# Optimization experiments

Measured on AMD Instinct MI355X. Metric: run time of the kernel, lower is better.

Reference implementation:

```python
import jax, jax.numpy as jnp
import numpy as np

B, L, DIN = 32, 512, 768
H, DH = 16, 48
DOUT = H * DH
NEG = 1e12


def setup_inputs() -> dict:
    key = jax.random.key(0)
    ks = jax.random.split(key, 8)
    lim = float(np.sqrt(6.0 / (DIN + DOUT)))  # xavier_uniform
    return {
        "Q_seq": jax.random.normal(ks[0], (B, L, DIN), jnp.float32),
        "K_seq": jax.random.normal(ks[1], (B, L, DIN), jnp.float32),
        "V_seq": jax.random.normal(ks[2], (B, L, DIN), jnp.float32),
        "WQ": jax.random.uniform(ks[3], (DIN, DOUT), jnp.float32, -lim, lim),
        "WK": jax.random.uniform(ks[4], (DIN, DOUT), jnp.float32, -lim, lim),
        "WV": jax.random.uniform(ks[5], (DIN, DOUT), jnp.float32, -lim, lim),
        "Q_len": jax.random.randint(ks[6], (B, 1), 0, L, jnp.int64),
        "V_len": jax.random.randint(ks[7], (B, 1), 0, L, jnp.int64),
    }


def reference(Q_seq, K_seq, V_seq, WQ, WK, WV, Q_len, V_len):
    b, l = Q_seq.shape[0], Q_seq.shape[1]
    # projections -> [B, H, L, DH]
    q = (Q_seq @ WQ).reshape(b, l, H, DH).transpose(0, 2, 1, 3)
    k = (K_seq @ WK).reshape(b, l, H, DH).transpose(0, 2, 1, 3)
    v = (V_seq @ WV).reshape(b, l, H, DH).transpose(0, 2, 1, 3)
    # scaled scores [B, H, Lq, Lk]
    A = jnp.einsum("bhqd,bhkd->bhqk", q, k) / jnp.sqrt(jnp.float32(DH))
    # key-length additive mask (original: scatter+cumsum == arange < len)
    mask_k = (jnp.arange(l) < V_len[:, 0][:, None]).astype(A.dtype)  # [B, Lk]
    A = A - (1.0 - mask_k)[:, None, None, :] * NEG
    # causal mask (mask_right=True): subtract on strictly upper triangle
    A = A - jnp.triu(jnp.ones((l, l), A.dtype), 1) * NEG
    A = jax.nn.softmax(A, axis=-1)
    # original quirk: O = A^T @ V  -> O[b,h,k,d] = sum_q A[b,h,q,k] V[b,h,q,d]
    O = jnp.einsum("bhqk,bhqd->bkhd", A, v).reshape(b, l, DOUT)
    # query-length multiplicative mask on output
    mask_q = (jnp.arange(l) < Q_len[:, 0][:, None]).astype(O.dtype)  # [B, L]
    return O * mask_q[:, :, None]
```

## Files before the change

kernel.cpp:

```cpp
#include <hip/hip_runtime.h>
#include <stdint.h>

#define B_    32
#define L_    512
#define DIN_  768
#define H_    16
#define DH_   48
#define DOUT_ 768
#define NHEADS (B_ * H_)
#define HEADELEMS (L_ * DH_)

typedef short bf16x8 __attribute__((ext_vector_type(8)));
typedef float f32x4  __attribute__((ext_vector_type(4)));

__device__ __forceinline__ uint16_t f2bf(float f) {
  uint32_t u = __float_as_uint(f);
  u += 0x7fffu + ((u >> 16) & 1u);
  return (uint16_t)(u >> 16);
}
__device__ __forceinline__ uint32_t pack2bf(float lo, float hi) {
  uint32_t a = __float_as_uint(lo);
  a += 0x7fffu + ((a >> 16) & 1u);
  uint32_t b = __float_as_uint(hi);
  b += 0x7fffu + ((b >> 16) & 1u);
  return (a >> 16) | (b & 0xffff0000u);
}
__device__ __forceinline__ void gload_lds16(const void* g, void* l) {
  __builtin_amdgcn_global_load_lds(
      (const __attribute__((address_space(1))) uint32_t*)g,
      (__attribute__((address_space(3))) uint32_t*)l, 16, 0, 0);
}
__device__ __forceinline__ bf16x8 lds_frag8(const uint16_t* p) {
  union { uint2 u[2]; bf16x8 v; } x;
  x.u[0] = *(const uint2*)(p);
  x.u[1] = *(const uint2*)(p + 4);
  return x.v;
}

__global__ void lens_kernel(const int* __restrict__ qlen_raw,
                            const int* __restrict__ vlen_raw,
                            int* __restrict__ lens) {
  __shared__ int is64[2];
  int t = threadIdx.x;
  if (t < 2) {
    const int* src = (t == 0) ? qlen_raw : vlen_raw;
    int o = 0;
    for (int i = 0; i < 16; ++i) o |= src[2 * i + 1];
    is64[t] = (o == 0) ? 1 : 0;
  }
  __syncthreads();
  int which = t >> 5;
  int i = t & 31;
  const int* src = which ? vlen_raw : qlen_raw;
  lens[t] = is64[which] ? src[2 * i] : src[i];
}

__global__ void wconv_kernel(const float* __restrict__ WQ,
                             const float* __restrict__ WK,
                             const float* __restrict__ WV,
                             uint16_t* __restrict__ Wt) {
  const int z = blockIdx.z;
  const float* W = (z == 0) ? WQ : (z == 1) ? WK : WV;
  uint16_t* dst = Wt + (size_t)z * DIN_ * DOUT_;
  const int n  = blockIdx.x * 256 + threadIdx.x;
  const int k4 = blockIdx.y * 4;
  float f0 = W[(size_t)(k4 + 0) * DOUT_ + n];
  float f1 = W[(size_t)(k4 + 1) * DOUT_ + n];
  float f2 = W[(size_t)(k4 + 2) * DOUT_ + n];
  float f3 = W[(size_t)(k4 + 3) * DOUT_ + n];
  uint2 p;
  p.x = pack2bf(f0, f1);
  p.y = pack2bf(f2, f3);
  *(uint2*)&dst[(size_t)n * DIN_ + k4] = p;
}

__global__ __launch_bounds__(512, 4) void mfma_proj(
    const float* __restrict__ Xq, const float* __restrict__ Xk,
    const float* __restrict__ Xv, const uint16_t* __restrict__ Wt,
    uint16_t* __restrict__ qh, uint16_t* __restrict__ kh,
    uint16_t* __restrict__ vh) {
  const int z = blockIdx.z;
  const float* X = (z == 0) ? Xq : (z == 1) ? Xk : Xv;
  uint16_t* dst  = (z == 0) ? qh : (z == 1) ? kh : vh;
  const uint16_t* W = Wt + (size_t)z * DIN_ * DOUT_;

  __shared__ uint16_t As[128][32];
  __shared__ uint16_t Bs[128][32];

  const int t  = threadIdx.x;
  const int m0 = blockIdx.x * 128;
  const int n0 = blockIdx.y * 128;

  const int ra = t >> 2;
  const int ca = (t & 3) * 8;
  const float* aptr = X + (size_t)(m0 + ra) * DIN_ + ca;

  const uint16_t* bptr = W + (size_t)(n0 + (t >> 2)) * DIN_ + (t & 3) * 8;
  void* ldsB = (char*)(&Bs[0][0]) + t * 16;

  const int w = t >> 6, lane = t & 63;
  const int wm = (w & 3) * 32, wn = (w >> 2) * 64;
  const int fr = lane & 15;
  const int quad = lane >> 4;

  f32x4 acc[2][4];
#pragma unroll
  for (int i = 0; i < 2; ++i)
#pragma unroll
    for (int j = 0; j < 4; ++j) acc[i][j] = f32x4{0.f, 0.f, 0.f, 0.f};

  for (int kt = 0; kt < DIN_ / 32; ++kt) {
    const int k0 = kt * 32;
    gload_lds16(bptr + k0, ldsB);
    float4 x0 = *(const float4*)(aptr + k0);
    float4 x1 = *(const float4*)(aptr + k0 + 4);
    uint4 pA;
    pA.x = pack2bf(x0.x, x0.y); pA.y = pack2bf(x0.z, x0.w);
    pA.z = pack2bf(x1.x, x1.y); pA.w = pack2bf(x1.z, x1.w);
    *(uint4*)&As[ra][ca] = pA;
    __syncthreads();

    bf16x8 af[2], bfr[4];
#pragma unroll
    for (int i = 0; i < 2; ++i)
      af[i]  = *(const bf16x8*)&As[wm + i * 16 + fr][quad * 8];
#pragma unroll
    for (int j = 0; j < 4; ++j)
      bfr[j] = *(const bf16x8*)&Bs[wn + j * 16 + fr][quad * 8];
#pragma unroll
    for (int mt = 0; mt < 2; ++mt)
#pragma unroll
      for (int nt = 0; nt < 4; ++nt)
        acc[mt][nt] = __builtin_amdgcn_mfma_f32_16x16x32_bf16(
            af[mt], bfr[nt], acc[mt][nt], 0, 0, 0);
    __syncthreads();
  }

#pragma unroll
  for (int mt = 0; mt < 2; ++mt) {
#pragma unroll
    for (int r = 0; r < 4; ++r) {
      const int m  = m0 + wm + mt * 16 + quad * 4 + r;
      const int bb = m >> 9;
      const int l  = m & 511;
#pragma unroll
      for (int nt = 0; nt < 4; ++nt) {
        const int n = n0 + wn + nt * 16 + fr;
        const int h = n / DH_;
        const int d = n - h * DH_;
        dst[(((size_t)bb * H_ + h) * L_ + l) * DH_ + d] = f2bf(acc[mt][nt][r]);
      }
    }
  }
}

__global__ __launch_bounds__(256, 2) void attn_mfma(
    const uint16_t* __restrict__ qh, const uint16_t* __restrict__ kh,
    const uint16_t* __restrict__ vh, const int* __restrict__ lens,
    float* __restrict__ out) {
  const int bh = blockIdx.x;
  const int b  = bh >> 4;
  const int h  = bh & 15;
  const int t    = threadIdx.x;
  const int w    = t >> 6;
  const int lane = t & 63;
  const int l15  = lane & 15;
  const int quad = lane >> 4;

  const int qlen = lens[b];
  const int vlen = lens[32 + b];
  const bool deg = (vlen == 0);
  const size_t head = (size_t)bh * HEADELEMS;

  __shared__ uint16_t Pt[4][128][36];
  __shared__ uint16_t Vt[48][36];
  __shared__ float    prt[4][32];
  __shared__ float    cmb[32];

  const uint16_t* qbase = qh + head;
  const uint16_t* kbase = kh + head;
  const uint16_t* vbase = vh + head;

  f32x4 Oacc[8][3];
#pragma unroll
  for (int i = 0; i < 8; ++i)
#pragma unroll
    for (int dt = 0; dt < 3; ++dt) Oacc[i][dt] = f32x4{0.f, 0.f, 0.f, 0.f};

  const float scale = 0.14433756729740643f;
  const int vq  = t & 31;
  const int vd4 = t >> 5;

  for (int g = 0; g < 16; ++g) {
    const int q0 = g * 32;
    const int lim = q0 + 31 - 16 * w;

    __syncthreads();

    {
      uint2 u = *(const uint2*)(vbase + (size_t)(q0 + vq) * DH_ + vd4 * 4);
      Vt[vd4 * 4 + 0][vq] = (uint16_t)(u.x);
      Vt[vd4 * 4 + 1][vq] = (uint16_t)(u.x >> 16);
      Vt[vd4 * 4 + 2][vq] = (uint16_t)(u.y);
      Vt[vd4 * 4 + 3][vq] = (uint16_t)(u.y >> 16);
      if (t < 128) {
        int d4b = 8 + (t >> 5);
        uint2 v = *(const uint2*)(vbase + (size_t)(q0 + vq) * DH_ + d4b * 4);
        Vt[d4b * 4 + 0][vq] = (uint16_t)(v.x);
        Vt[d4b * 4 + 1][vq] = (uint16_t)(v.x >> 16);
        Vt[d4b * 4 + 2][vq] = (uint16_t)(v.y);
        Vt[d4b * 4 + 3][vq] = (uint16_t)(v.y >> 16);
      }
    }

    bf16x8 aq[2][2];
#pragma unroll
    for (int mt = 0; mt < 2; ++mt) {
      const uint16_t* qp = qbase + (size_t)(q0 + mt * 16 + l15) * DH_;
      aq[mt][0] = *(const bf16x8*)(qp + quad * 8);
      bf16x8 zz = {0, 0, 0, 0, 0, 0, 0, 0};
      aq[mt][1] = zz;
      if (quad < 2) aq[mt][1] = *(const bf16x8*)(qp + 32 + quad * 8);
    }

    float lrun[2][4];
#pragma unroll
    for (int mt = 0; mt < 2; ++mt)
#pragma unroll
      for (int r = 0; r < 4; ++r) lrun[mt][r] = 0.0f;

#pragma unroll
    for (int i = 0; i < 8; ++i) {
      if (64 * i > lim) continue;
      const int kb = 64 * i + 16 * w;
      f32x4 s0 = {0.f, 0.f, 0.f, 0.f};
      f32x4 s1 = {0.f, 0.f, 0.f, 0.f};
      if (!deg) {
        const uint16_t* kp = kbase + (size_t)(kb + l15) * DH_;
        bf16x8 bk0 = *(const bf16x8*)(kp + quad * 8);
        bf16x8 bk1 = {0, 0, 0, 0, 0, 0, 0, 0};
        if (quad < 2) bk1 = *(const bf16x8*)(kp + 32 + quad * 8);
        s0 = __builtin_amdgcn_mfma_f32_16x16x32_bf16(aq[0][0], bk0, s0, 0, 0, 0);
        s0 = __builtin_amdgcn_mfma_f32_16x16x32_bf16(aq[0][1], bk1, s0, 0, 0, 0);
        s1 = __builtin_amdgcn_mfma_f32_16x16x32_bf16(aq[1][0], bk0, s1, 0, 0, 0);
        s1 = __builtin_amdgcn_mfma_f32_16x16x32_bf16(aq[1][1], bk1, s1, 0, 0, 0);
      }
      const int kc  = kb + l15;
      const int row = i * 16 + l15;
#pragma unroll
      for (int mt = 0; mt < 2; ++mt) {
        f32x4 sv = (mt == 0) ? s0 : s1;
        float p4[4];
#pragma unroll
        for (int r = 0; r < 4; ++r) {
          const int qrow = q0 + mt * 16 + quad * 4 + r;
          float e;
          if (deg) {
            e = (kc <= qrow) ? 1.0f : 0.0f;
          } else {
            e = (kc < vlen && kc <= qrow) ? __expf(sv[r] * scale) : 0.0f;
          }
          lrun[mt][r] += e;
          p4[r] = e;
        }
        const int col = mt * 16 + quad * 4;
        *(uint32_t*)&Pt[w][row][col]     = pack2bf(p4[0], p4[1]);
        *(uint32_t*)&Pt[w][row][col + 2] = pack2bf(p4[2], p4[3]);
      }
    }

#pragma unroll
    for (int mt = 0; mt < 2; ++mt)
#pragma unroll
      for (int r = 0; r < 4; ++r) {
        float l = lrun[mt][r];
#pragma unroll
        for (int off = 1; off < 16; off <<= 1) l += __shfl_xor(l, off, 64);
        lrun[mt][r] = l;
      }
    if (l15 == 0) {
#pragma unroll
      for (int mt = 0; mt < 2; ++mt)
#pragma unroll
        for (int r = 0; r < 4; ++r)
          prt[w][mt * 16 + quad * 4 + r] = lrun[mt][r];
    }
    __syncthreads();

    if (t < 32) cmb[t] = 1.0f / (prt[0][t] + prt[1][t] + prt[2][t] + prt[3][t]);
    __syncthreads();

#pragma unroll
    for (int j = 0; j < 6; ++j) {
      const int idx = t + j * 256;
      const int d = idx >> 5, q = idx & 31;
      float f = __uint_as_float((uint32_t)Vt[d][q] << 16) * cmb[q];
      Vt[d][q] = f2bf(f);
    }
    __syncthreads();

    bf16x8 bv[3];
#pragma unroll
    for (int dt = 0; dt < 3; ++dt)
      bv[dt] = lds_frag8(&Vt[dt * 16 + l15][quad * 8]);
#pragma unroll
    for (int i = 0; i < 8; ++i) {
      if (64 * i > lim) continue;
      bf16x8 ap = lds_frag8(&Pt[w][i * 16 + l15][quad * 8]);
#pragma unroll
      for (int dt = 0; dt < 3; ++dt)
        Oacc[i][dt] = __builtin_amdgcn_mfma_f32_16x16x32_bf16(
            ap, bv[dt], Oacc[i][dt], 0, 0, 0);
    }
  }

#pragma unroll
  for (int i = 0; i < 8; ++i) {
#pragma unroll
    for (int r = 0; r < 4; ++r) {
      const int k_abs = 64 * i + 16 * w + quad * 4 + r;
      const float msk = (k_abs < qlen) ? 1.0f : 0.0f;
      float* orow = out + (size_t)(b * L_ + k_abs) * DOUT_ + h * DH_;
#pragma unroll
      for (int dt = 0; dt < 3; ++dt)
        orow[dt * 16 + l15] = Oacc[i][dt][r] * msk;
    }
  }
}

extern "C" void kernel_launch(void* const* d_in, const int* in_sizes, int n_in,
                              void* d_out, int out_size, void* d_ws, size_t ws_size,
                              hipStream_t stream) {
  const float* Qs  = (const float*)d_in[0];
  const float* Kse = (const float*)d_in[1];
  const float* Vs  = (const float*)d_in[2];
  const float* WQ  = (const float*)d_in[3];
  const float* WK  = (const float*)d_in[4];
  const float* WV  = (const float*)d_in[5];
  const int*   Qlen = (const int*)d_in[6];
  const int*   Vlen = (const int*)d_in[7];
  float* out = (float*)d_out;

  char* ws = (char*)d_ws;
  int* lens = (int*)ws;
  uint16_t* qh = (uint16_t*)(ws + 256);
  uint16_t* kh = qh + (size_t)B_ * H_ * L_ * DH_;
  uint16_t* vh = kh + (size_t)B_ * H_ * L_ * DH_;
  uint16_t* Wt = vh + (size_t)B_ * H_ * L_ * DH_;

  lens_kernel<<<1, 64, 0, stream>>>(Qlen, Vlen, lens);
  wconv_kernel<<<dim3(3, 192, 3), 256, 0, stream>>>(WQ, WK, WV, Wt);
  mfma_proj<<<dim3(16384 / 128, DOUT_ / 128, 3), 512, 0, stream>>>(
      Qs, Kse, Vs, Wt, qh, kh, vh);
  attn_mfma<<<NHEADS, 256, 0, stream>>>(qh, kh, vh, lens, out);
}
```

Before: 350.8 us.

## Double K-tile depth with XOR-swizzled LDS in projection; atomic row-sum reduction in attention

The projection GEMM now stages 64-wide K tiles instead of 32 and uses an XOR swizzle on the LDS layout for A and B to avoid bank conflicts. This halves the number of barrier pairs per GEMM. The attention kernel replaces the per-wave partial-sum array and separate combine step with LDS atomicAdd into a single row-sum array, removing one barrier per query group. Launch-bound occupancy hints rise for both kernels, which may force register spilling.

```diff
diff --git a/kernel.cpp b/kernel.cpp
--- a/kernel.cpp
+++ b/kernel.cpp
@@ -74,7 +74,7 @@
   *(uint2*)&dst[(size_t)n * DIN_ + k4] = p;
 }
 
-__global__ __launch_bounds__(512, 4) void mfma_proj(
+__global__ __launch_bounds__(512, 6) void mfma_proj(
     const float* __restrict__ Xq, const float* __restrict__ Xk,
     const float* __restrict__ Xv, const uint16_t* __restrict__ Wt,
     uint16_t* __restrict__ qh, uint16_t* __restrict__ kh,
@@ -84,19 +84,26 @@
   uint16_t* dst  = (z == 0) ? qh : (z == 1) ? kh : vh;
   const uint16_t* W = Wt + (size_t)z * DIN_ * DOUT_;
 
-  __shared__ uint16_t As[128][32];
-  __shared__ uint16_t Bs[128][32];
+  __shared__ uint16_t As[128][64];
+  __shared__ uint16_t Bs[128][64];
 
   const int t  = threadIdx.x;
   const int m0 = blockIdx.x * 128;
   const int n0 = blockIdx.y * 128;
 
-  const int ra = t >> 2;
-  const int ca = (t & 3) * 8;
-  const float* aptr = X + (size_t)(m0 + ra) * DIN_ + ca;
-
-  const uint16_t* bptr = W + (size_t)(n0 + (t >> 2)) * DIN_ + (t & 3) * 8;
-  void* ldsB = (char*)(&Bs[0][0]) + t * 16;
+  const int ra  = t >> 2;
+  const int ja0 = (t & 3) * 2;
+  const float* aptr = X + (size_t)(m0 + ra) * DIN_ + ja0 * 8;
+  const int sa0 = (ja0 ^ (ra & 7)) * 8;
+  const int sa1 = ((ja0 + 1) ^ (ra & 7)) * 8;
+
+  const int c0b = t;
+  const int c1b = t + 512;
+  const int r0b = c0b >> 3, j0b = c0b & 7, s0b = (j0b ^ (r0b & 7)) * 8;
+  const int r1b = c1b >> 3, j1b = c1b & 7, s1b = (j1b ^ (r1b & 7)) * 8;
+  const uint16_t* bsrc0 = W + (size_t)(n0 + r0b) * DIN_ + s0b;
+  const uint16_t* bsrc1 = W + (size_t)(n0 + r1b) * DIN_ + s1b;
+  char* ldsB = (char*)(&Bs[0][0]);
 
   const int w = t >> 6, lane = t & 63;
   const int wm = (w & 3) * 32, wn = (w >> 2) * 64;
@@ -109,30 +116,43 @@
 #pragma unroll
     for (int j = 0; j < 4; ++j) acc[i][j] = f32x4{0.f, 0.f, 0.f, 0.f};
 
-  for (int kt = 0; kt < DIN_ / 32; ++kt) {
-    const int k0 = kt * 32;
-    gload_lds16(bptr + k0, ldsB);
+  for (int kt = 0; kt < DIN_ / 64; ++kt) {
+    const int k0 = kt * 64;
+    gload_lds16(bsrc0 + k0, ldsB + c0b * 16);
+    gload_lds16(bsrc1 + k0, ldsB + c1b * 16);
     float4 x0 = *(const float4*)(aptr + k0);
     float4 x1 = *(const float4*)(aptr + k0 + 4);
-    uint4 pA;
+    float4 x2 = *(const float4*)(aptr + k0 + 8);
+    float4 x3 = *(const float4*)(aptr + k0 + 12);
+    uint4 pA, pB;
     pA.x = pack2bf(x0.x, x0.y); pA.y = pack2bf(x0.z, x0.w);
     pA.z = pack2bf(x1.x, x1.y); pA.w = pack2bf(x1.z, x1.w);
-    *(uint4*)&As[ra][ca] = pA;
-    __syncthreads();
-
-    bf16x8 af[2], bfr[4];
-#pragma unroll
-    for (int i = 0; i < 2; ++i)
-      af[i]  = *(const bf16x8*)&As[wm + i * 16 + fr][quad * 8];
-#pragma unroll
-    for (int j = 0; j < 4; ++j)
-      bfr[j] = *(const bf16x8*)&Bs[wn + j * 16 + fr][quad * 8];
-#pragma unroll
-    for (int mt = 0; mt < 2; ++mt)
-#pragma unroll
-      for (int nt = 0; nt < 4; ++nt)
-        acc[mt][nt] = __builtin_amdgcn_mfma_f32_16x16x32_bf16(
-            af[mt], bfr[nt], acc[mt][nt], 0, 0, 0);
+    pB.x = pack2bf(x2.x, x2.y); pB.y = pack2bf(x2.z, x2.w);
+    pB.z = pack2bf(x3.x, x3.y); pB.w = pack2bf(x3.z, x3.w);
+    *(uint4*)&As[ra][sa0] = pA;
+    *(uint4*)&As[ra][sa1] = pB;
+    __syncthreads();
+
+#pragma unroll
+    for (int ks = 0; ks < 2; ++ks) {
+      bf16x8 af[2], bfr[4];
+#pragma unroll
+      for (int i = 0; i < 2; ++i) {
+        const int row = wm + i * 16 + fr;
+        af[i] = *(const bf16x8*)&As[row][((4 * ks + quad) ^ (row & 7)) * 8];
+      }
+#pragma unroll
+      for (int j = 0; j < 4; ++j) {
+        const int row = wn + j * 16 + fr;
+        bfr[j] = *(const bf16x8*)&Bs[row][((4 * ks + quad) ^ (row & 7)) * 8];
+      }
+#pragma unroll
+      for (int mt = 0; mt < 2; ++mt)
+#pragma unroll
+        for (int nt = 0; nt < 4; ++nt)
+          acc[mt][nt] = __builtin_amdgcn_mfma_f32_16x16x32_bf16(
+              af[mt], bfr[nt], acc[mt][nt], 0, 0, 0);
+    }
     __syncthreads();
   }
 
@@ -154,7 +174,7 @@
   }
 }
 
-__global__ __launch_bounds__(256, 2) void attn_mfma(
+__global__ __launch_bounds__(256, 3) void attn_mfma(
     const uint16_t* __restrict__ qh, const uint16_t* __restrict__ kh,
     const uint16_t* __restrict__ vh, const int* __restrict__ lens,
     float* __restrict__ out) {
@@ -174,8 +194,7 @@
 
   __shared__ uint16_t Pt[4][128][36];
   __shared__ uint16_t Vt[48][36];
-  __shared__ float    prt[4][32];
-  __shared__ float    cmb[32];
+  __shared__ float    Ls[32];
 
   const uint16_t* qbase = qh + head;
   const uint16_t* kbase = kh + head;
@@ -190,6 +209,8 @@
   const float scale = 0.14433756729740643f;
   const int vq  = t & 31;
   const int vd4 = t >> 5;
+
+  if (t < 32) Ls[t] = 0.0f;
 
   for (int g = 0; g < 16; ++g) {
     const int q0 = g * 32;
@@ -283,21 +304,20 @@
       for (int mt = 0; mt < 2; ++mt)
 #pragma unroll
         for (int r = 0; r < 4; ++r)
-          prt[w][mt * 16 + quad * 4 + r] = lrun[mt][r];
-    }
-    __syncthreads();
-
-    if (t < 32) cmb[t] = 1.0f / (prt[0][t] + prt[1][t] + prt[2][t] + prt[3][t]);
+          atomicAdd(&Ls[mt * 16 + quad * 4 + r], lrun[mt][r]);
+    }
     __syncthreads();
 
 #pragma unroll
     for (int j = 0; j < 6; ++j) {
       const int idx = t + j * 256;
       const int d = idx >> 5, q = idx & 31;
-      float f = __uint_as_float((uint32_t)Vt[d][q] << 16) * cmb[q];
+      float f = __uint_as_float((uint32_t)Vt[d][q] << 16) * (1.0f / Ls[q]);
       Vt[d][q] = f2bf(f);
     }
     __syncthreads();
+
+    if (t < 32) Ls[t] = 0.0f;
 
     bf16x8 bv[3];
 #pragma unroll
```

After: 405.1 us. +15.5%, slower.
